# Optimization experiments

Hardware: AMD Instinct MI355X
Metric: run time of the kernel (lower is better)

The kernel has to match this reference:

```python
import jax, jax.numpy as jnp
import numpy as np

NUM_CLASSES = 100
EPS = 1e-8  # torch F.cosine_similarity default eps


def setup_inputs() -> dict:
    key = jax.random.key(0)
    k1, k2 = jax.random.split(key)
    feat = jax.random.normal(k1, (100000, 512), dtype=jnp.float32)
    label = jax.random.randint(k2, (100000,), 0, NUM_CLASSES, dtype=jnp.int64)
    return {"feat": feat, "label": label}


def reference(feat, label):
    # Per-class mean (segment mean) -- replaces the Python loop over classes.
    sums = jax.ops.segment_sum(feat, label, num_segments=NUM_CLASSES)          # [C, D]
    counts = jax.ops.segment_sum(jnp.ones_like(label, dtype=feat.dtype), label,
                                 num_segments=NUM_CLASSES)                      # [C]
    means = sums / jnp.maximum(counts, 1.0)[:, None]                            # [C, D]

    # Only the gathered (own-class) column of the sim matrix is returned,
    # so compute cos(feat[i], means[label[i]]) directly.
    cent = means[label]                                                         # [N, D]
    dot = jnp.sum(feat * cent, axis=-1)                                         # [N]
    n_feat = jnp.maximum(jnp.linalg.norm(feat, axis=-1), EPS)
    n_cent = jnp.maximum(jnp.linalg.norm(cent, axis=-1), EPS)
    return dot / (n_feat * n_cent)
```

## Files before the change

### kernel.cpp

```cpp
#include <hip/hip_runtime.h>

#define NCLS 100
#define DIM  512
#define EPSV 1e-8f

#define DSPL  4
#define CH    192
#define BATCH 16
#define SCALE 262144.0f

__global__ __launch_bounds__(256, 4) void sum_kernel(const float* __restrict__ feat,
                                                     const int* __restrict__ label,
                                                     int* __restrict__ S, int n) {
    __shared__ int acc[NCLS * 128];
    const int tid = threadIdx.x;
    const int ds  = blockIdx.x;
    const int ch  = blockIdx.y;

    for (int i = tid; i < NCLS * 128; i += 256) acc[i] = 0;
    __syncthreads();

    const int rpc  = (n + CH - 1) / CH;
    const int rows = min(rpc, n - ch * rpc);
    const int r0   = ch * rpc;
    const int w    = tid >> 6;
    const int lane = tid & 63;
    const int lo   = (rows * w) >> 2;
    const int hi   = (rows * (w + 1)) >> 2;
    const float* f0 = feat + (size_t)ds * 128 + lane;

    int r = lo;
    for (; r + BATCH <= hi; r += BATCH) {
        float va[BATCH], vb[BATCH];
        #pragma unroll
        for (int k = 0; k < BATCH; ++k) {
            const float* p = f0 + (size_t)(r0 + r + k) * DIM;
            va[k] = p[0];
            vb[k] = p[64];
        }
        const int myl = label[r0 + r + (lane & (BATCH - 1))];
        #pragma unroll
        for (int k = 0; k < BATCH; ++k) {
            const int c = __shfl(myl, k, 64);
            int* a = &acc[c * 128 + lane];
            atomicAdd(a,      __float2int_rn(va[k] * SCALE));
            atomicAdd(a + 64, __float2int_rn(vb[k] * SCALE));
        }
    }
    for (; r < hi; ++r) {
        const int c = label[r0 + r];
        const float* p = f0 + (size_t)(r0 + r) * DIM;
        int* a = &acc[c * 128 + lane];
        atomicAdd(a,      __float2int_rn(p[0]  * SCALE));
        atomicAdd(a + 64, __float2int_rn(p[64] * SCALE));
    }
    __syncthreads();

    for (int i = tid; i < NCLS * 128; i += 256) {
        const int c = i >> 7;
        const int j = i & 127;
        atomicAdd(&S[(size_t)c * DIM + ds * 128 + j], acc[i]);
    }
}

__global__ __launch_bounds__(512) void norm_kernel(const int* __restrict__ S,
                                                   float* __restrict__ mhat) {
    const int c = blockIdx.x;
    const int t = threadIdx.x;
    const float v = (float)S[(size_t)c * DIM + t];

    float ss = v * v;
    #pragma unroll
    for (int o = 32; o; o >>= 1) ss += __shfl_down(ss, o, 64);
    __shared__ float red[8];
    if ((t & 63) == 0) red[t >> 6] = ss;
    __syncthreads();
    float tot = 0.f;
    #pragma unroll
    for (int k = 0; k < 8; ++k) tot += red[k];
    const float q = (tot > 0.f) ? (1.0f / sqrtf(tot)) : 0.0f;
    mhat[(size_t)c * DIM + t] = v * q;
}

__global__ __launch_bounds__(256) void cos_kernel(const float* __restrict__ feat,
                                                  const int* __restrict__ label,
                                                  const float* __restrict__ mhat,
                                                  float* __restrict__ out, int n) {
    const int lane = threadIdx.x & 63;
    const int wv   = threadIdx.x >> 6;
    const int cl   = lane >> 4;
    const int t    = lane & 15;

    const int row = blockIdx.x * 16 + wv * 4 + cl;
    const bool ok = row < n;
    const int rr = ok ? row : (n - 1);

    const int c = label[rr];
    const float4* f4 = (const float4*)(feat + (size_t)rr * DIM);
    const float4* m4 = (const float4*)(mhat + (size_t)c  * DIM);

    float4 a[8], b[8];
    #pragma unroll
    for (int j = 0; j < 8; ++j) a[j] = f4[t + 16 * j];
    #pragma unroll
    for (int j = 0; j < 8; ++j) b[j] = m4[t + 16 * j];

    float dot = 0.0f, nf = 0.0f;
    #pragma unroll
    for (int j = 0; j < 8; ++j) {
        dot += a[j].x * b[j].x + a[j].y * b[j].y + a[j].z * b[j].z + a[j].w * b[j].w;
        nf  += a[j].x * a[j].x + a[j].y * a[j].y + a[j].z * a[j].z + a[j].w * a[j].w;
    }

    #pragma unroll
    for (int off = 8; off; off >>= 1) {
        dot += __shfl_xor(dot, off, 64);
        nf  += __shfl_xor(nf,  off, 64);
    }
    if (t == 0 && ok) {
        out[row] = dot / fmaxf(sqrtf(nf), EPSV);
    }
}

extern "C" void kernel_launch(void* const* d_in, const int* in_sizes, int n_in,
                              void* d_out, int out_size, void* d_ws, size_t ws_size,
                              hipStream_t stream) {
    const float* feat  = (const float*)d_in[0];
    const int*   label = (const int*)d_in[1];
    float*       out   = (float*)d_out;
    const int n = in_sizes[0] / DIM;

    int*   S    = (int*)d_ws;
    float* mhat = (float*)(S + NCLS * DIM);

    hipMemsetAsync(S, 0, NCLS * DIM * sizeof(int), stream);

    dim3 sg(DSPL, CH);
    sum_kernel<<<sg, 256, 0, stream>>>(feat, label, S, n);
    norm_kernel<<<NCLS, 512, 0, stream>>>(S, mhat);
    cos_kernel<<<(n + 15) / 16, 256, 0, stream>>>(feat, label, mhat, out, n);
}
```

Before: 335.5 us.

## Split sum kernel into 64-wide column slices and double-buffer row batch loads

```diff
diff --git a/kernel.cpp b/kernel.cpp
--- a/kernel.cpp
+++ b/kernel.cpp
@@ -4,63 +4,71 @@
 #define DIM  512
 #define EPSV 1e-8f
 
-#define DSPL  4
+#define DSPL  8
 #define CH    192
 #define BATCH 16
 #define SCALE 262144.0f
 
-__global__ __launch_bounds__(256, 4) void sum_kernel(const float* __restrict__ feat,
+__global__ __launch_bounds__(256, 6) void sum_kernel(const float* __restrict__ feat,
                                                      const int* __restrict__ label,
                                                      int* __restrict__ S, int n) {
-    __shared__ int acc[NCLS * 128];
+    __shared__ int acc[NCLS * 64];
     const int tid = threadIdx.x;
     const int ds  = blockIdx.x;
     const int ch  = blockIdx.y;
 
-    for (int i = tid; i < NCLS * 128; i += 256) acc[i] = 0;
+    for (int i = tid; i < NCLS * 64; i += 256) acc[i] = 0;
     __syncthreads();
 
     const int rpc  = (n + CH - 1) / CH;
-    const int rows = min(rpc, n - ch * rpc);
     const int r0   = ch * rpc;
+    const int rows = min(rpc, n - r0);
     const int w    = tid >> 6;
     const int lane = tid & 63;
-    const int lo   = (rows * w) >> 2;
-    const int hi   = (rows * (w + 1)) >> 2;
-    const float* f0 = feat + (size_t)ds * 128 + lane;
+    const int lo   = (rows * w) / 4;
+    const int hi   = (rows * (w + 1)) / 4;
+    const float* fb = feat + (size_t)ds * 64 + lane;
 
-    int r = lo;
-    for (; r + BATCH <= hi; r += BATCH) {
-        float va[BATCH], vb[BATCH];
+    float vA[BATCH], vB[BATCH];
+    int mylA = 0, mylB = 0;
+
+    auto loadA = [&](int rb) {
+        mylA = label[r0 + rb + (lane & (BATCH - 1))];
         #pragma unroll
-        for (int k = 0; k < BATCH; ++k) {
-            const float* p = f0 + (size_t)(r0 + r + k) * DIM;
-            va[k] = p[0];
-            vb[k] = p[64];
-        }
-        const int myl = label[r0 + r + (lane & (BATCH - 1))];
+        for (int k = 0; k < BATCH; ++k)
+            vA[k] = fb[(size_t)(r0 + rb + k) * DIM];
+    };
+    auto loadB = [&](int rb) {
+        mylB = label[r0 + rb + (lane & (BATCH - 1))];
+        #pragma unroll
+        for (int k = 0; k < BATCH; ++k)
+            vB[k] = fb[(size_t)(r0 + rb + k) * DIM];
+    };
+    auto proc = [&](int myl, float (&v)[BATCH]) {
         #pragma unroll
         for (int k = 0; k < BATCH; ++k) {
             const int c = __shfl(myl, k, 64);
-            int* a = &acc[c * 128 + lane];
-            atomicAdd(a,      __float2int_rn(va[k] * SCALE));
-            atomicAdd(a + 64, __float2int_rn(vb[k] * SCALE));
+            atomicAdd(&acc[c * 64 + lane], __float2int_rn(v[k] * SCALE));
         }
+    };
+
+    const int nb = (hi - lo) / BATCH;
+    if (nb > 0) {
+        loadA(lo);
+        for (int ib = 0; ib + 1 < nb; ++ib) {
+            if (ib & 1) { loadA(lo + (ib + 1) * BATCH); proc(mylB, vB); }
+            else        { loadB(lo + (ib + 1) * BATCH); proc(mylA, vA); }
+        }
+        if ((nb - 1) & 1) proc(mylB, vB); else proc(mylA, vA);
     }
-    for (; r < hi; ++r) {
+    for (int r = lo + nb * BATCH; r < hi; ++r) {
         const int c = label[r0 + r];
-        const float* p = f0 + (size_t)(r0 + r) * DIM;
-        int* a = &acc[c * 128 + lane];
-        atomicAdd(a,      __float2int_rn(p[0]  * SCALE));
-        atomicAdd(a + 64, __float2int_rn(p[64] * SCALE));
+        atomicAdd(&acc[c * 64 + lane], __float2int_rn(fb[(size_t)(r0 + r) * DIM] * SCALE));
     }
     __syncthreads();
 
-    for (int i = tid; i < NCLS * 128; i += 256) {
-        const int c = i >> 7;
-        const int j = i & 127;
-        atomicAdd(&S[(size_t)c * DIM + ds * 128 + j], acc[i]);
-    }
+    for (int i = tid; i < NCLS * 64; i += 256)
+        atomicAdd(&S[(size_t)(i >> 6) * DIM + ds * 64 + (i & 63)], acc[i]);
 }
 
 __global__ __launch_bounds__(512) void norm_kernel(const int* __restrict__ S,
```

New measurement: 327.2 us. -2.5%, faster.
